# Kernel tuning notes

Hardware: AMD Instinct MI355X
Metric: run time of the kernel (lower is better)

The kernel has to match this reference:

```python
import jax, jax.numpy as jnp
import numpy as np
import math

D_MODEL = 1024
N_HEADS = 16
D_HEAD = D_MODEL // N_HEADS

def setup_inputs() -> dict:
    key = jax.random.key(0)
    k1, k2, k3 = jax.random.split(key, 3)
    x = jax.random.normal(k1, (4, 2048, D_MODEL), dtype=jnp.float32)
    # torch Linear weights are [out, in]; kept in that layout, applied as x @ W.T
    s = 1.0 / math.sqrt(D_MODEL)
    W_qkv = jax.random.uniform(k2, (3 * D_MODEL, D_MODEL), jnp.float32, -s, s)
    W_proj = jax.random.uniform(k3, (D_MODEL, D_MODEL), jnp.float32, -s, s)
    return {"x": x, "W_qkv": W_qkv, "W_proj": W_proj}

def reference(x, W_qkv, W_proj):
    B, T, d = x.shape
    qkv = x @ W_qkv.T  # [B,T,3d]
    q, k, v = jnp.split(qkv, 3, axis=-1)
    def split(t):
        return t.reshape(B, T, N_HEADS, D_HEAD).transpose(0, 2, 1, 3)  # [B,H,T,Dh]
    q, k, v = split(q), split(k), split(v)
    scores = jnp.einsum('bhqd,bhkd->bhqk', q, k) / math.sqrt(D_HEAD)
    mask = jnp.tril(jnp.ones((T, T), dtype=bool))
    scores = jnp.where(mask, scores, -jnp.inf)
    attn = jax.nn.softmax(scores, axis=-1)
    out = jnp.einsum('bhqk,bhkd->bhqd', attn, v)  # [B,H,T,Dh]
    out = out.transpose(0, 2, 1, 3).reshape(B, T, d)
    return out @ W_proj.T
```

## Files before the change

### kernel.cpp

```cpp
#include <hip/hip_runtime.h>
#include <hip/hip_bf16.h>
#include <math.h>

typedef __attribute__((ext_vector_type(8))) short short8;
typedef __attribute__((ext_vector_type(4))) float f32x4;
typedef __attribute__((ext_vector_type(16))) float f32x16;
typedef __attribute__((ext_vector_type(2))) unsigned uint2v;
typedef __attribute__((ext_vector_type(4))) unsigned uint4v;

#define B_  4
#define T_  2048
#define DM  1024
#define NH  16
#define DH  64
#define BH  (B_*NH)
#define M_  (B_*T_)

#define QSCALE 0.18033688011112042f

static __device__ __forceinline__ short f2bf(float f) {
  unsigned u = __float_as_uint(f);
  unsigned r = (u + 0x7fff + ((u >> 16) & 1)) >> 16;
  return (short)r;
}

static __device__ __forceinline__ unsigned cvtpk(float lo, float hi) {
  unsigned r;
  asm("v_cvt_pk_bf16_f32 %0, %1, %2" : "=v"(r) : "v"(lo), "v"(hi));
  return r;
}

static __device__ __forceinline__ float expasm(float x) {
  float r;
  asm("v_exp_f32 %0, %1" : "=v"(r) : "v"(x));
  return r;
}

static __device__ __forceinline__ void gload_lds16(const void* g, void* l) {
  __builtin_amdgcn_global_load_lds((const __attribute__((address_space(1))) void*)g,
                                   (__attribute__((address_space(3))) void*)l, 16, 0, 0);
}

__global__ void k_cvt3(const float4* __restrict__ x, const float4* __restrict__ wq,
                       const float4* __restrict__ wp, ushort4* __restrict__ ox,
                       ushort4* __restrict__ oq, ushort4* __restrict__ op) {
  const int n1 = M_ * DM / 4, n2 = 3 * DM * DM / 4, n3 = DM * DM / 4;
  int i = blockIdx.x * 256 + threadIdx.x;
  const float4* src;
  ushort4* dst;
  int j = i;
  if (i < n1) { src = x; dst = ox; }
  else if (i < n1 + n2) { src = wq; dst = oq; j = i - n1; }
  else if (i < n1 + n2 + n3) { src = wp; dst = op; j = i - n1 - n2; }
  else return;
  float4 v = src[j];
  ushort4 o;
  o.x = (ushort)f2bf(v.x); o.y = (ushort)f2bf(v.y);
  o.z = (ushort)f2bf(v.z); o.w = (ushort)f2bf(v.w);
  dst[j] = o;
}

#define GEMM_STAGE(SRCA, SRCB, dA, dB, m0_, n0_, k0_)                          \
  {                                                                            \
    _Pragma("unroll")                                                          \
    for (int i = 0; i < 4; ++i) {                                              \
      int lin = i * 256 + tid;                                                 \
      int row = lin >> 3, pseg = lin & 7;                                      \
      int gseg = pseg ^ (row & 7);                                             \
      gload_lds16(&SRCA[(size_t)((m0_) + row) * DM + (k0_) + gseg * 8],        \
                  &(dA)[lin * 8]);                                             \
    }                                                                          \
    _Pragma("unroll")                                                          \
    for (int i = 0; i < 4; ++i) {                                              \
      int lin = i * 256 + tid;                                                 \
      int row = lin >> 3, pseg = lin & 7;                                      \
      int gseg = pseg ^ (row & 7);                                             \
      gload_lds16(&SRCB[(size_t)((n0_) + row) * DM + (k0_) + gseg * 8],        \
                  &(dB)[lin * 8]);                                             \
    }                                                                          \
  }

#define GEMM_COMPUTE(pA, pB)                                                   \
  {                                                                            \
    _Pragma("unroll")                                                          \
    for (int kk = 0; kk < 2; ++kk) {                                           \
      short8 aF[4], bF[4];                                                     \
      _Pragma("unroll")                                                        \
      for (int m = 0; m < 4; ++m)                                              \
        aF[m] = *(const short8*)&(pA)[(wr * 64 + m * 16 + fr) * 64 +           \
                                      (((kk * 4 + fq) ^ (fr & 7)) * 8)];       \
      _Pragma("unroll")                                                        \
      for (int n = 0; n < 4; ++n)                                              \
        bF[n] = *(const short8*)&(pB)[(wc * 64 + n * 16 + fr) * 64 +           \
                                      (((kk * 4 + fq) ^ (fr & 7)) * 8)];       \
      __builtin_amdgcn_s_setprio(1);                                           \
      _Pragma("unroll")                                                        \
      for (int m = 0; m < 4; ++m)                                              \
        _Pragma("unroll")                                                      \
        for (int n = 0; n < 4; ++n)                                            \
          acc[m][n] = __builtin_amdgcn_mfma_f32_16x16x32_bf16(aF[m], bF[n],    \
                                                              acc[m][n], 0, 0, 0); \
      __builtin_amdgcn_s_setprio(0);                                           \
    }                                                                          \
  }

#define GEMM_KLOOP(SRCA, SRCB, m0_, n0_)                                       \
  GEMM_STAGE(SRCA, SRCB, sA0, sB0, m0_, n0_, 0);                               \
  {                                                                            \
    _Pragma("unroll 1")                                                        \
    for (int t = 0; t < 16; ++t) {                                             \
      short* pA = (t & 1) ? sA1 : sA0;                                         \
      short* pB = (t & 1) ? sB1 : sB0;                                         \
      if (t < 15) {                                                            \
        short* nA = (t & 1) ? sA0 : sA1;                                       \
        short* nB = (t & 1) ? sB0 : sB1;                                       \
        GEMM_STAGE(SRCA, SRCB, nA, nB, m0_, n0_, (t + 1) * 64);                \
        asm volatile("s_waitcnt vmcnt(8)" ::: "memory");                       \
      } else {                                                                 \
        asm volatile("s_waitcnt vmcnt(0)" ::: "memory");                       \
      }                                                                        \
      __builtin_amdgcn_s_barrier();                                            \
      __builtin_amdgcn_sched_barrier(0);                                       \
      GEMM_COMPUTE(pA, pB);                                                    \
      asm volatile("" ::: "memory");                                           \
      __builtin_amdgcn_s_barrier();                                            \
    }                                                                          \
  }

__global__ __launch_bounds__(256, 2) void k_gemm_qkv(
    const short* __restrict__ A,
    const short* __restrict__ W,
    short* __restrict__ Qb, short* __restrict__ Kb, short* __restrict__ Vtb) {
  const int tid = threadIdx.x;
  const int w = tid >> 6, l = tid & 63;
  const int wr = w >> 1, wc = w & 1;
  const int fq = l >> 4, fr = l & 15;
  const int m0 = blockIdx.x * 128;
  const int n0 = blockIdx.y * 128;

  __shared__ short lds[32768];
  short* sA0 = lds;
  short* sA1 = lds + 8192;
  short* sB0 = lds + 16384;
  short* sB1 = lds + 24576;

  f32x4 acc[4][4] = {};
  GEMM_KLOOP(A, W, m0, n0);
  __syncthreads();

  short* sE = lds;
  const int part = n0 >> 10;
  const int b = m0 >> 11, tloc = m0 & 2047;

  if (part < 2) {
    const float sc = part ? 1.0f : QSCALE;
#pragma unroll
    for (int m = 0; m < 4; ++m)
#pragma unroll
      for (int n = 0; n < 4; ++n)
#pragma unroll
        for (int j = 0; j < 4; ++j)
          sE[(wr * 64 + m * 16 + fq * 4 + j) * 136 + wc * 64 + n * 16 + fr] =
              f2bf(acc[m][n][j] * sc);
    __syncthreads();
    short* dst = part ? Kb : Qb;
    const int h0 = (n0 & 1023) >> 6;
#pragma unroll
    for (int v = 0; v < 8; ++v) {
      int vid = v * 256 + tid;
      int row = vid >> 4, seg = vid & 15;
      short8 val = *(const short8*)&sE[row * 136 + seg * 8];
      int h = h0 + (seg >> 3), dh0 = (seg & 7) * 8;
      *(short8*)&dst[(((size_t)(b * NH + h) * T_ + tloc + row)) * DH + dh0] = val;
    }
  } else {
#pragma unroll
    for (int m = 0; m < 4; ++m)
#pragma unroll
      for (int n = 0; n < 4; ++n) {
        uint2v pk;
        pk[0] = cvtpk(acc[m][n][0], acc[m][n][1]);
        pk[1] = cvtpk(acc[m][n][2], acc[m][n][3]);
        *(uint2v*)&sE[(wc * 64 + n * 16 + fr) * 136 + wr * 64 + m * 16 + fq * 4] = pk;
      }
    __syncthreads();
    const int h0 = (n0 & 1023) >> 6;
#pragma unroll
    for (int v = 0; v < 8; ++v) {
      int vid = v * 256 + tid;
      int col = vid >> 4, seg = vid & 15;
      short8 val = *(const short8*)&sE[col * 136 + seg * 8];
      int h = h0 + (col >> 6), dh = col & 63;
      *(short8*)&Vtb[(((size_t)(b * NH + h) * DH + dh)) * T_ + tloc + seg * 8] = val;
    }
  }
}

__global__ __launch_bounds__(256, 2) void k_gemm_proj(
    const short* __restrict__ A,
    const short* __restrict__ W,
    float* __restrict__ C) {
  const int tid = threadIdx.x;
  const int w = tid >> 6, l = tid & 63;
  const int wr = w >> 1, wc = w & 1;
  const int fq = l >> 4, fr = l & 15;
  const int m0 = blockIdx.x * 128;
  const int n0 = blockIdx.y * 128;

  __shared__ short lds[32768];
  short* sA0 = lds;
  short* sA1 = lds + 8192;
  short* sB0 = lds + 16384;
  short* sB1 = lds + 24576;

  f32x4 acc[4][4] = {};
  GEMM_KLOOP(A, W, m0, n0);

#pragma unroll
  for (int m = 0; m < 4; ++m) {
    int row0 = m0 + wr * 64 + m * 16 + fq * 4;
#pragma unroll
    for (int n = 0; n < 4; ++n) {
      int col = n0 + wc * 64 + n * 16 + fr;
#pragma unroll
      for (int j = 0; j < 4; ++j)
        C[(size_t)(row0 + j) * DM + col] = acc[m][n][j];
    }
  }
}

__global__ __launch_bounds__(512, 4) void k_attn12(
    const short* __restrict__ Qb,
    const short* __restrict__ Kb,
    const short* __restrict__ Vtb,
    short* __restrict__ Ob) {
  const int tid = threadIdx.x;
  const int w = tid >> 6, l = tid & 63;
  const int lq = l & 31, hi = l >> 5;
  const int id = blockIdx.x;
  const int x = id >> 6;
  const int qt = (x < 4) ? (7 - x) : (x - 4);
  const int bh = id & 63;
  const int b = bh >> 4, h = bh & 15;

  __shared__ short lds[32768];

  auto STAGE = [&](int slot, int kt) {
    int row = tid >> 3, pseg = tid & 7;
    int gseg = pseg ^ (row & 7);
    gload_lds16(&Kb[((size_t)bh * T_ + kt * 64 + row) * DH + gseg * 8],
                &lds[slot * 8192 + tid * 8]);
    gload_lds16(&Vtb[((size_t)bh * DH + row) * T_ + kt * 64 + gseg * 8],
                &lds[slot * 8192 + 4096 + tid * 8]);
  };

  const int nkt = 4 * qt + 4;
  const int q0 = qt * 256 + w * 32;
  const int qg = q0 + lq;

  short8 qf[4];
#pragma unroll
  for (int c = 0; c < 4; ++c)
    qf[c] = *(const short8*)&Qb[((size_t)bh * T_ + qg) * DH + c * 16 + hi * 8];
  asm volatile("s_waitcnt vmcnt(0)" ::: "memory");

  float lsum = 0.f;
  f32x16 oacc[2] = {};

  auto CSUB = [&](int kt, const int koff) {
    f32x16 a0 = {}, a1 = {};
    __builtin_amdgcn_s_setprio(1);
#pragma unroll
    for (int c = 0; c < 4; ++c) {
      short8 kf0 = *(const short8*)&lds[koff + (lq) * 64 + (((2 * c + hi) ^ (lq & 7)) * 8)];
      short8 kf1 = *(const short8*)&lds[koff + (32 + lq) * 64 + (((2 * c + hi) ^ (lq & 7)) * 8)];
      a0 = __builtin_amdgcn_mfma_f32_32x32x16_bf16(kf0, qf[c], a0, 0, 0, 0);
      a1 = __builtin_amdgcn_mfma_f32_32x32x16_bf16(kf1, qf[c], a1, 0, 0, 0);
    }
    __builtin_amdgcn_s_setprio(0);

    if (kt * 64 + 63 > q0) {
#pragma unroll
      for (int r = 0; r < 16; ++r) {
        int kg0 = kt * 64 + (r & 3) + 8 * (r >> 2) + 4 * hi;
        if (kg0 > qg) a0[r] = -1e30f;
        if (kg0 + 32 > qg) a1[r] = -1e30f;
      }
    }

#pragma unroll
    for (int r = 0; r < 16; ++r) {
      a0[r] = expasm(a0[r]);
      a1[r] = expasm(a1[r]);
    }
    {
      float t[8];
#pragma unroll
      for (int i = 0; i < 8; ++i)
        t[i] = (a0[2 * i] + a0[2 * i + 1]) + (a1[2 * i] + a1[2 * i + 1]);
      float u0 = (t[0] + t[1]) + (t[2] + t[3]);
      float u1 = (t[4] + t[5]) + (t[6] + t[7]);
      lsum += u0 + u1;
    }

    short8 pb[4];
#pragma unroll
    for (int st = 0; st < 2; ++st) {
      const f32x16& P = st ? a1 : a0;
      unsigned x0 = cvtpk(P[0], P[1]);
      unsigned x1 = cvtpk(P[2], P[3]);
      unsigned y0 = cvtpk(P[4], P[5]);
      unsigned y1 = cvtpk(P[6], P[7]);
      uint2v r0 = __builtin_amdgcn_permlane32_swap(x0, y0, false, false);
      uint2v r1 = __builtin_amdgcn_permlane32_swap(x1, y1, false, false);
      unsigned x2 = cvtpk(P[8], P[9]);
      unsigned x3 = cvtpk(P[10], P[11]);
      unsigned y2 = cvtpk(P[12], P[13]);
      unsigned y3 = cvtpk(P[14], P[15]);
      uint2v r2 = __builtin_amdgcn_permlane32_swap(x2, y2, false, false);
      uint2v r3 = __builtin_amdgcn_permlane32_swap(x3, y3, false, false);
      uint4v ta, tb;
      ta[0] = r0[0]; ta[1] = r1[0]; ta[2] = r0[1]; ta[3] = r1[1];
      tb[0] = r2[0]; tb[1] = r3[0]; tb[2] = r2[1]; tb[3] = r3[1];
      pb[st * 2 + 0] = __builtin_bit_cast(short8, ta);
      pb[st * 2 + 1] = __builtin_bit_cast(short8, tb);
    }

    __builtin_amdgcn_s_setprio(1);
#pragma unroll
    for (int dt = 0; dt < 2; ++dt) {
#pragma unroll
      for (int c = 0; c < 4; ++c) {
        short8 vf = *(const short8*)&lds[koff + 4096 + (dt * 32 + lq) * 64 +
                                         (((2 * c + hi) ^ (lq & 7)) * 8)];
        oacc[dt] = __builtin_amdgcn_mfma_f32_32x32x16_bf16(vf, pb[c], oacc[dt], 0, 0, 0);
      }
    }
    __builtin_amdgcn_s_setprio(0);
  };

  STAGE(0, 0);
  if (nkt > 1) STAGE(1, 1);
#pragma unroll 1
  for (int t = 0; t < nkt; ++t) {
    if (t + 2 < nkt) {
      STAGE((t + 2) & 3, t + 2);
      asm volatile("s_waitcnt vmcnt(4)" ::: "memory");
    } else if (t + 1 < nkt) {
      asm volatile("s_waitcnt vmcnt(2)" ::: "memory");
    } else {
      asm volatile("s_waitcnt vmcnt(0)" ::: "memory");
    }
    __builtin_amdgcn_s_barrier();
    __builtin_amdgcn_sched_barrier(0);
    if (t * 64 <= q0 + 31) CSUB(t, (t & 3) * 8192);
  }

  lsum += __shfl_xor(lsum, 32);
  __syncthreads();
  short* sO = lds + w * 2304;
  float inv = 1.0f / lsum;
#pragma unroll
  for (int dt = 0; dt < 2; ++dt)
#pragma unroll
    for (int r = 0; r < 16; r += 2) {
      int dl = dt * 32 + (r & 3) + 8 * (r >> 2) + 4 * hi;
      *(unsigned*)&sO[lq * 72 + dl] = cvtpk(oacc[dt][r] * inv, oacc[dt][r + 1] * inv);
    }
  asm volatile("s_waitcnt lgkmcnt(0)" ::: "memory");
  __builtin_amdgcn_sched_barrier(0);
  {
    int qr = l >> 1, hf = l & 1;
    const int tg = q0 + qr;
#pragma unroll
    for (int ss = 0; ss < 4; ++ss) {
      short8 v = *(const short8*)&sO[qr * 72 + hf * 32 + ss * 8];
      *(short8*)&Ob[((size_t)(b * T_) + tg) * DM + h * 64 + hf * 32 + ss * 8] = v;
    }
  }
}

extern "C" void kernel_launch(void* const* d_in, const int* in_sizes, int n_in,
                              void* d_out, int out_size, void* d_ws, size_t ws_size,
                              hipStream_t stream) {
  const float* x     = (const float*)d_in[0];
  const float* Wqkv  = (const float*)d_in[1];
  const float* Wproj = (const float*)d_in[2];
  float* out = (float*)d_out;

  short* ws = (short*)d_ws;
  short* xbf   = ws;
  short* wqkvb = xbf + (size_t)M_ * DM;
  short* wprjb = wqkvb + (size_t)3 * DM * DM;
  short* Qb    = wprjb + (size_t)DM * DM;
  short* Kb    = Qb + (size_t)BH * T_ * DH;
  short* Vtb   = Kb + (size_t)BH * T_ * DH;
  short* Ob    = Vtb + (size_t)BH * T_ * DH;

  const int ncv = (M_ * DM + 3 * DM * DM + DM * DM) / 4;
  k_cvt3<<<(ncv + 255) / 256, 256, 0, stream>>>(
      (const float4*)x, (const float4*)Wqkv, (const float4*)Wproj,
      (ushort4*)xbf, (ushort4*)wqkvb, (ushort4*)wprjb);

  k_gemm_qkv<<<dim3(M_ / 128, 3 * DM / 128), 256, 0, stream>>>(xbf, wqkvb, Qb, Kb, Vtb);
  k_attn12<<<512, 512, 0, stream>>>(Qb, Kb, Vtb, Ob);
  k_gemm_proj<<<dim3(M_ / 128, DM / 128), 256, 0, stream>>>(Ob, wprjb, out);
}
```

Before: 135.7 us.

## Replace QKV GEMM with 256x256-tile, 8-wave kernel using split-K-half pipelining

```diff
diff --git a/kernel.cpp b/kernel.cpp
--- a/kernel.cpp
+++ b/kernel.cpp
@@ -58,6 +58,161 @@
   o.x = (ushort)f2bf(v.x); o.y = (ushort)f2bf(v.y);
   o.z = (ushort)f2bf(v.z); o.w = (ushort)f2bf(v.w);
   dst[j] = o;
+}
+
+__global__ __launch_bounds__(512, 2) void k_gemm_qkv2(
+    const short* __restrict__ A,
+    const short* __restrict__ W,
+    short* __restrict__ Qb, short* __restrict__ Kb, short* __restrict__ Vtb) {
+  const int tid = threadIdx.x;
+  const int w = tid >> 6, l = tid & 63;
+  const int wm = w >> 2, wn = w & 3;
+  const int fq = l >> 4, fr = l & 15;
+  const int m0 = blockIdx.x * 256;
+  const int n0 = blockIdx.y * 256;
+
+  __shared__ short lds[65536];
+
+  auto SA = [&](int slot, int kt, int kh) {
+#pragma unroll
+    for (int i = 0; i < 2; ++i) {
+      int c = i * 512 + tid;
+      int row = c >> 2, seg = c & 3;
+      gload_lds16(&A[(size_t)(m0 + row) * DM + kt * 64 + kh * 32 + seg * 8],
+                  &lds[slot * 32768 + kh * 8192 + c * 8]);
+    }
+  };
+  auto SB = [&](int slot, int kt, int kh) {
+#pragma unroll
+    for (int i = 0; i < 2; ++i) {
+      int c = i * 512 + tid;
+      int row = c >> 2, seg = c & 3;
+      gload_lds16(&W[(size_t)(n0 + row) * DM + kt * 64 + kh * 32 + seg * 8],
+                  &lds[slot * 32768 + 16384 + kh * 8192 + c * 8]);
+    }
+  };
+
+  f32x4 acc[8][4] = {};
+  short8 bF[4];
+
+  auto RUN_PHASE = [&](int soff, int kh, int mh, int waitn, auto stg) {
+    short8 aF[4];
+#pragma unroll
+    for (int m_ = 0; m_ < 4; ++m_)
+      aF[m_] = *(const short8*)&lds[soff + kh * 8192 +
+                                    (wm * 128 + (mh * 4 + m_) * 16 + fr) * 32 + fq * 8];
+    if (mh == 0) {
+#pragma unroll
+      for (int n_ = 0; n_ < 4; ++n_)
+        bF[n_] = *(const short8*)&lds[soff + 16384 + kh * 8192 +
+                                      (wn * 64 + n_ * 16 + fr) * 32 + fq * 8];
+    }
+    stg();
+    if (waitn == 4) asm volatile("s_waitcnt vmcnt(4)" ::: "memory");
+    else if (waitn == 0) asm volatile("s_waitcnt vmcnt(0)" ::: "memory");
+    __builtin_amdgcn_s_barrier();
+    asm volatile("s_waitcnt lgkmcnt(0)" ::: "memory");
+    __builtin_amdgcn_sched_barrier(0);
+    __builtin_amdgcn_s_setprio(1);
+#pragma unroll
+    for (int m_ = 0; m_ < 4; ++m_)
+#pragma unroll
+      for (int n_ = 0; n_ < 4; ++n_)
+        acc[mh * 4 + m_][n_] = __builtin_amdgcn_mfma_f32_16x16x32_bf16(
+            aF[m_], bF[n_], acc[mh * 4 + m_][n_], 0, 0, 0);
+    __builtin_amdgcn_s_setprio(0);
+    __builtin_amdgcn_s_barrier();
+  };
+
+  SA(0, 0, 0); SB(0, 0, 0); SA(0, 0, 1); SB(0, 0, 1);
+  asm volatile("s_waitcnt vmcnt(4)" ::: "memory");
+  __builtin_amdgcn_s_barrier();
+
+#pragma unroll 1
+  for (int it = 0; it < 8; ++it) {
+    const int t0 = 2 * it;
+    RUN_PHASE(0, 0, 0, -1, [&]{ SA(1, t0 + 1, 0); });
+    RUN_PHASE(0, 0, 1,  4, [&]{ SB(1, t0 + 1, 0); });
+    RUN_PHASE(0, 1, 0, -1, [&]{ SA(1, t0 + 1, 1); });
+    RUN_PHASE(0, 1, 1,  4, [&]{ SB(1, t0 + 1, 1); });
+    if (it < 7) {
+      RUN_PHASE(32768, 0, 0, -1, [&]{ SA(0, t0 + 2, 0); });
+      RUN_PHASE(32768, 0, 1,  4, [&]{ SB(0, t0 + 2, 0); });
+      RUN_PHASE(32768, 1, 0, -1, [&]{ SA(0, t0 + 2, 1); });
+      RUN_PHASE(32768, 1, 1,  4, [&]{ SB(0, t0 + 2, 1); });
+    } else {
+      RUN_PHASE(32768, 0, 0, -1, [&]{});
+      RUN_PHASE(32768, 0, 1,  0, [&]{});
+      RUN_PHASE(32768, 1, 0, -1, [&]{});
+      RUN_PHASE(32768, 1, 1, -1, [&]{});
+    }
+  }
+
+  __syncthreads();
+  short* sE = lds;
+  const int part = n0 >> 10;
+  const int b = m0 >> 11, tloc = m0 & 2047;
+  const int h0 = (n0 & 1023) >> 6;
+
+  if (part < 2) {
+    const float sc = (part == 0) ? QSCALE : 1.0f;
+    short* dst = part ? Kb : Qb;
+#pragma unroll
+    for (int P = 0; P < 2; ++P) {
+      if (wm == P) {
+#pragma unroll
+        for (int mh = 0; mh < 2; ++mh)
+#pragma unroll
+          for (int m_ = 0; m_ < 4; ++m_)
+#pragma unroll
+            for (int n_ = 0; n_ < 4; ++n_)
+#pragma unroll
+              for (int j = 0; j < 4; ++j)
+                sE[((mh * 4 + m_) * 16 + fq * 4 + j) * 264 + wn * 64 + n_ * 16 + fr] =
+                    f2bf(acc[mh * 4 + m_][n_][j] * sc);
+      }
+      __syncthreads();
+#pragma unroll
+      for (int v = 0; v < 8; ++v) {
+        int vid = v * 512 + tid;
+        int row = vid >> 5, seg = vid & 31;
+        short8 val = *(const short8*)&sE[row * 264 + seg * 8];
+        int h = h0 + (seg >> 3), dh0 = (seg & 7) * 8;
+        *(short8*)&dst[(((size_t)(b * NH + h) * T_ + tloc + P * 128 + row)) * DH + dh0] = val;
+      }
+      __syncthreads();
+    }
+  } else {
+#pragma unroll
+    for (int P = 0; P < 2; ++P) {
+      if ((wn >> 1) == P) {
+#pragma unroll
+        for (int mh = 0; mh < 2; ++mh)
+#pragma unroll
+          for (int m_ = 0; m_ < 4; ++m_)
+#pragma unroll
+            for (int n_ = 0; n_ < 4; ++n_) {
+              uint2v pk;
+              pk[0] = cvtpk(acc[mh * 4 + m_][n_][0], acc[mh * 4 + m_][n_][1]);
+              pk[1] = cvtpk(acc[mh * 4 + m_][n_][2], acc[mh * 4 + m_][n_][3]);
+              int cl = (wn & 1) * 64 + n_ * 16 + fr;
+              int rowbase = wm * 128 + (mh * 4 + m_) * 16 + fq * 4;
+              *(uint2v*)&sE[cl * 264 + rowbase] = pk;
+            }
+      }
+      __syncthreads();
+#pragma unroll
+      for (int v = 0; v < 8; ++v) {
+        int vid = v * 512 + tid;
+        int cl = vid >> 5, seg = vid & 31;
+        short8 val = *(const short8*)&sE[cl * 264 + seg * 8];
+        int gcol = P * 128 + cl;
+        int h = h0 + (gcol >> 6), dh = gcol & 63;
+        *(short8*)&Vtb[(((size_t)(b * NH + h) * DH + dh)) * T_ + tloc + seg * 8] = val;
+      }
+      __syncthreads();
+    }
+  }
 }
 
 #define GEMM_STAGE(SRCA, SRCB, dA, dB, m0_, n0_, k0_)                          \
@@ -127,75 +282,6 @@
     }                                                                          \
   }
 
-__global__ __launch_bounds__(256, 2) void k_gemm_qkv(
-    const short* __restrict__ A,
-    const short* __restrict__ W,
-    short* __restrict__ Qb, short* __restrict__ Kb, short* __restrict__ Vtb) {
-  const int tid = threadIdx.x;
-  const int w = tid >> 6, l = tid & 63;
-  const int wr = w >> 1, wc = w & 1;
-  const int fq = l >> 4, fr = l & 15;
-  const int m0 = blockIdx.x * 128;
-  const int n0 = blockIdx.y * 128;
-
-  __shared__ short lds[32768];
-  short* sA0 = lds;
-  short* sA1 = lds + 8192;
-  short* sB0 = lds + 16384;
-  short* sB1 = lds + 24576;
-
-  f32x4 acc[4][4] = {};
-  GEMM_KLOOP(A, W, m0, n0);
-  __syncthreads();
-
-  short* sE = lds;
-  const int part = n0 >> 10;
-  const int b = m0 >> 11, tloc = m0 & 2047;
-
-  if (part < 2) {
-    const float sc = part ? 1.0f : QSCALE;
-#pragma unroll
-    for (int m = 0; m < 4; ++m)
-#pragma unroll
-      for (int n = 0; n < 4; ++n)
-#pragma unroll
-        for (int j = 0; j < 4; ++j)
-          sE[(wr * 64 + m * 16 + fq * 4 + j) * 136 + wc * 64 + n * 16 + fr] =
-              f2bf(acc[m][n][j] * sc);
-    __syncthreads();
-    short* dst = part ? Kb : Qb;
-    const int h0 = (n0 & 1023) >> 6;
-#pragma unroll
-    for (int v = 0; v < 8; ++v) {
-      int vid = v * 256 + tid;
-      int row = vid >> 4, seg = vid & 15;
-      short8 val = *(const short8*)&sE[row * 136 + seg * 8];
-      int h = h0 + (seg >> 3), dh0 = (seg & 7) * 8;
-      *(short8*)&dst[(((size_t)(b * NH + h) * T_ + tloc + row)) * DH + dh0] = val;
-    }
-  } else {
-#pragma unroll
-    for (int m = 0; m < 4; ++m)
-#pragma unroll
-      for (int n = 0; n < 4; ++n) {
-        uint2v pk;
-        pk[0] = cvtpk(acc[m][n][0], acc[m][n][1]);
-        pk[1] = cvtpk(acc[m][n][2], acc[m][n][3]);
-        *(uint2v*)&sE[(wc * 64 + n * 16 + fr) * 136 + wr * 64 + m * 16 + fq * 4] = pk;
-      }
-    __syncthreads();
-    const int h0 = (n0 & 1023) >> 6;
-#pragma unroll
-    for (int v = 0; v < 8; ++v) {
-      int vid = v * 256 + tid;
-      int col = vid >> 4, seg = vid & 15;
-      short8 val = *(const short8*)&sE[col * 136 + seg * 8];
-      int h = h0 + (col >> 6), dh = col & 63;
-      *(short8*)&Vtb[(((size_t)(b * NH + h) * DH + dh)) * T_ + tloc + seg * 8] = val;
-    }
-  }
-}
-
 __global__ __launch_bounds__(256, 2) void k_gemm_proj(
     const short* __restrict__ A,
     const short* __restrict__ W,
@@ -402,7 +488,7 @@
       (const float4*)x, (const float4*)Wqkv, (const float4*)Wproj,
       (ushort4*)xbf, (ushort4*)wqkvb, (ushort4*)wprjb);
 
-  k_gemm_qkv<<<dim3(M_ / 128, 3 * DM / 128), 256, 0, stream>>>(xbf, wqkvb, Qb, Kb, Vtb);
+  k_gemm_qkv2<<<dim3(M_ / 256, 3 * DM / 256), 512, 0, stream>>>(xbf, wqkvb, Qb, Kb, Vtb);
   k_attn12<<<512, 512, 0, stream>>>(Qb, Kb, Vtb, Ob);
   k_gemm_proj<<<dim3(M_ / 128, DM / 128), 256, 0, stream>>>(Ob, wprjb, out);
 }
```

Measured after the change: 431.3 us. 218% more time.
